# Kernel optimization log

Measured on AMD Instinct MI355X. Metric: run time of the kernel, lower is better.

Reference implementation:

```python
import jax, jax.numpy as jnp
import numpy as np

B, Q, D = 4, 8192, 256
L, P = 2, 8
H0 = W0 = 128
H1 = W1 = 64
EPS = 1e-5


def _bilinear_sample(feat, gx, gy):
    """grid_sample bilinear, padding_mode='border', align_corners=False.
    feat: (B, D, H, W); gx, gy: (B, N) in [-1, 1]. Returns (B, N, D)."""
    b, d, h, w = feat.shape
    # unnormalize (align_corners=False)
    x = ((gx + 1.0) * w - 1.0) * 0.5
    y = ((gy + 1.0) * h - 1.0) * 0.5
    # border padding: clamp coords into valid range
    x = jnp.clip(x, 0.0, w - 1.0)
    y = jnp.clip(y, 0.0, h - 1.0)
    x0 = jnp.floor(x)
    y0 = jnp.floor(y)
    wx = x - x0
    wy = y - y0
    x0i = x0.astype(jnp.int32)
    y0i = y0.astype(jnp.int32)
    x1i = jnp.minimum(x0i + 1, w - 1)
    y1i = jnp.minimum(y0i + 1, h - 1)
    fhw = feat.reshape(b, d, h * w)  # (B, D, H*W)

    def gather(iy, ix):
        idx = iy * w + ix  # (B, N)
        return jnp.take_along_axis(fhw, idx[:, None, :], axis=2)  # (B, D, N)

    v00 = gather(y0i, x0i)
    v01 = gather(y0i, x1i)
    v10 = gather(y1i, x0i)
    v11 = gather(y1i, x1i)
    wxb = wx[:, None, :]
    wyb = wy[:, None, :]
    top = v00 * (1.0 - wxb) + v01 * wxb
    bot = v10 * (1.0 - wxb) + v11 * wxb
    out = top * (1.0 - wyb) + bot * wyb  # (B, D, N)
    return out.transpose(0, 2, 1)  # (B, N, D)


def setup_inputs() -> dict:
    key = jax.random.key(0)
    ks = jax.random.split(key, 12)
    s = 0.02
    return {
        "q": jax.random.normal(ks[0], (B, Q, D), jnp.float32),
        "map0": jax.random.normal(ks[1], (B, D, H0, W0), jnp.float32),
        "map1": jax.random.normal(ks[2], (B, D, H1, W1), jnp.float32),
        "base_ref": jax.random.uniform(ks[3], (B, L, 2), jnp.float32),
        "Wrd": jax.random.normal(ks[4], (D, L * 2), jnp.float32) * s,
        "brd": jax.random.normal(ks[5], (L * 2,), jnp.float32) * s,
        "Woff": jax.random.normal(ks[6], (D, L * P * 2), jnp.float32) * s,
        "boff": jax.random.normal(ks[7], (L * P * 2,), jnp.float32) * 1.5,
        "Wattn": jax.random.normal(ks[8], (D, L * P), jnp.float32) * s,
        "battn": jax.random.normal(ks[9], (L * P,), jnp.float32) * s,
        "Wout": jax.random.normal(ks[10], (D, D), jnp.float32) * s,
        "bout": jax.random.normal(ks[11], (D,), jnp.float32) * s,
    }


def reference(q, map0, map1, base_ref, Wrd, brd, Woff, boff, Wattn, battn, Wout, bout):
    b, qn, d = q.shape
    maps = [map0, map1]
    # per-level reference points, refined through inverse-sigmoid space
    base = jnp.clip(base_ref, EPS, 1.0 - EPS)[:, None, :, :]  # (B, 1, L, 2)
    logit_base = jnp.log(base / (1.0 - base))
    ref_delta = (q @ Wrd + brd).reshape(b, qn, L, 2)
    ref = jax.nn.sigmoid(logit_base + ref_delta)  # (B, Q, L, 2)
    offsets = (q @ Woff + boff).reshape(b, qn, L, P, 2)
    attn_logits = (q @ Wattn + battn).reshape(b, qn, L * P)
    attn = jax.nn.softmax(attn_logits, axis=-1).reshape(b, qn, L, P)

    out = jnp.zeros((b, qn, d), jnp.float32)
    for level, feat in enumerate(maps):
        h, w = feat.shape[2], feat.shape[3]
        normalizer = jnp.array([w, h], jnp.float32)
        loc = ref[:, :, level, None, :] + offsets[:, :, level] / normalizer  # (B,Q,P,2)
        if level == 1:
            loc = jnp.stack([loc[..., 0], jnp.remainder(loc[..., 1], 1.0)], axis=-1)
        loc = loc * 2.0 - 1.0
        gx = loc[..., 0].reshape(b, qn * P)
        gy = loc[..., 1].reshape(b, qn * P)
        samp = _bilinear_sample(feat, gx, gy).reshape(b, qn, P, d)
        out = out + jnp.sum(samp * attn[:, :, level, :, None], axis=2)
    return out @ Wout + bout
```

## Files before the change

kernel.cpp:

```cpp
#include <hip/hip_runtime.h>
#include <hip/hip_bf16.h>

#define BQ 4
#define QN 8192
#define DD 256
#define LL 2
#define H0c 128
#define W0c 128
#define H1c 64
#define W1c 64
#define EPSF 1e-5f

typedef unsigned short ushort_t;
typedef __attribute__((ext_vector_type(8))) short short8;
typedef __attribute__((ext_vector_type(8))) unsigned short ushortx8;
typedef __attribute__((ext_vector_type(4))) unsigned short ushortx4;
typedef __attribute__((ext_vector_type(4))) float floatx4;
typedef __attribute__((ext_vector_type(4))) _Float16 half4;

static __device__ __forceinline__ float lo16f(unsigned int d) {
    union { unsigned int u; float f; } x; x.u = d << 16; return x.f;
}
static __device__ __forceinline__ float hi16f(unsigned int d) {
    union { unsigned int u; float f; } x; x.u = d & 0xFFFF0000u; return x.f;
}
static __device__ __forceinline__ unsigned short f2bf(float f) {
    __hip_bfloat16 h = __float2bfloat16(f);
    return __builtin_bit_cast(unsigned short, h);
}

#define PT0 4096
#define PT1 1024
#define PTW 16
__global__ __launch_bounds__(256) void prep(const float* __restrict__ map0, const float* __restrict__ map1,
                                            const float* __restrict__ Wout,
                                            const float* __restrict__ Wrd, const float* __restrict__ brd,
                                            const float* __restrict__ Woff, const float* __restrict__ boff,
                                            const float* __restrict__ Wattn, const float* __restrict__ battn,
                                            __hip_bfloat16* __restrict__ mapT0, __hip_bfloat16* __restrict__ mapT1,
                                            __hip_bfloat16* __restrict__ WoutT,
                                            float* __restrict__ Wall, float* __restrict__ bias64) {
    __shared__ float tile[64][65];
    int blk = blockIdx.x;
    int tid = threadIdx.x;
    const float* in; __hip_bfloat16* outp; int HW, b, c0, hw0;
    if (blk < PT0) {
        int l = blk; b = l >> 10; int r = l & 1023;
        c0 = (r >> 8) << 6; hw0 = (r & 255) << 6;
        in = map0; outp = mapT0; HW = H0c * W0c;
    } else if (blk < PT0 + PT1) {
        int l = blk - PT0; b = l >> 8; int r = l & 255;
        c0 = (r >> 6) << 6; hw0 = (r & 63) << 6;
        in = map1; outp = mapT1; HW = H1c * W1c;
    } else if (blk < PT0 + PT1 + PTW) {
        int l = blk - PT0 - PT1; b = 0;
        c0 = (l >> 2) << 6; hw0 = (l & 3) << 6;
        in = Wout; outp = WoutT; HW = DD;
    } else {
        int l = blk - PT0 - PT1 - PTW;
        int idx = l * 256 + tid;
        int k = idx >> 6, c = idx & 63;
        float v = (c < 4)  ? Wrd[k * 4 + c]
                : (c < 36) ? Woff[k * 32 + (c - 4)]
                : (c < 52) ? Wattn[k * 16 + (c - 36)]
                : 0.f;
        Wall[idx] = v;
        if (idx < 64) {
            float bv = (idx < 4)  ? brd[idx]
                     : (idx < 36) ? boff[idx - 4]
                     : (idx < 52) ? battn[idx - 36]
                     : 0.f;
            bias64[idx] = bv;
        }
        return;
    }
    const float* inb = in + (size_t)b * DD * HW + (size_t)c0 * HW + hw0;
    __hip_bfloat16* outb = outp + (size_t)b * DD * HW + (size_t)hw0 * DD + c0;

    int row = tid >> 2;
    int q16 = (tid & 3) * 16;
#pragma unroll
    for (int j = 0; j < 4; j++) {
        float4 v = *(const float4*)(inb + (size_t)row * HW + q16 + j * 4);
        tile[row][q16 + j * 4 + 0] = v.x;
        tile[row][q16 + j * 4 + 1] = v.y;
        tile[row][q16 + j * 4 + 2] = v.z;
        tile[row][q16 + j * 4 + 3] = v.w;
    }
    __syncthreads();

    int hwr = tid >> 4;
    int c4 = (tid & 15) * 4;
#pragma unroll
    for (int jj = 0; jj < 4; jj++) {
        int rr = hwr + jj * 16;
        ushortx4 o;
        o[0] = f2bf(tile[c4 + 0][rr]);
        o[1] = f2bf(tile[c4 + 1][rr]);
        o[2] = f2bf(tile[c4 + 2][rr]);
        o[3] = f2bf(tile[c4 + 3][rr]);
        *(ushortx4*)((ushort_t*)outb + (size_t)rr * DD + c4) = o;
    }
}

__global__ __launch_bounds__(256) void proj_desc(const float* __restrict__ q,
                                                 const float* __restrict__ Wall,
                                                 const float* __restrict__ bias64,
                                                 const float* __restrict__ base_ref,
                                                 int2* __restrict__ dsi,
                                                 half4* __restrict__ dsw) {
    __shared__ float As[32][68];
    __shared__ float Bs[32][64];
    __shared__ float prs[64][68];
    int tid = threadIdx.x;
    int tx = tid & 15, ty = tid >> 4;
    int m0 = blockIdx.x * 64;
    float acc[4][4] = {};

    for (int kt = 0; kt < DD; kt += 32) {
#pragma unroll
        for (int j = 0; j < 8; j++) {
            int e = tid + 256 * j;
            int r = e >> 5, k = e & 31;
            As[k][r] = q[(size_t)(m0 + r) * DD + kt + k];
        }
#pragma unroll
        for (int j = 0; j < 8; j++) {
            int e = tid + 256 * j;
            int k = e >> 6, nn = e & 63;
            Bs[k][nn] = Wall[(size_t)(kt + k) * 64 + nn];
        }
        __syncthreads();
#pragma unroll
        for (int k = 0; k < 32; k++) {
            const float4 a4 = *(const float4*)&As[k][ty * 4];
            const float4 b4 = *(const float4*)&Bs[k][tx * 4];
            acc[0][0] += a4.x * b4.x; acc[0][1] += a4.x * b4.y; acc[0][2] += a4.x * b4.z; acc[0][3] += a4.x * b4.w;
            acc[1][0] += a4.y * b4.x; acc[1][1] += a4.y * b4.y; acc[1][2] += a4.y * b4.z; acc[1][3] += a4.y * b4.w;
            acc[2][0] += a4.z * b4.x; acc[2][1] += a4.z * b4.y; acc[2][2] += a4.z * b4.z; acc[2][3] += a4.z * b4.w;
            acc[3][0] += a4.w * b4.x; acc[3][1] += a4.w * b4.y; acc[3][2] += a4.w * b4.z; acc[3][3] += a4.w * b4.w;
        }
        __syncthreads();
    }

    float4 bias = *(const float4*)&bias64[tx * 4];
#pragma unroll
    for (int i = 0; i < 4; i++) {
        float4 v;
        v.x = acc[i][0] + bias.x;
        v.y = acc[i][1] + bias.y;
        v.z = acc[i][2] + bias.z;
        v.w = acc[i][3] + bias.w;
        *(float4*)&prs[ty * 4 + i][tx * 4] = v;
    }
    __syncthreads();

    int ql = tid >> 2, sq = tid & 3;
    int n = m0 + ql, b = n >> 13;
    const float* p = prs[ql];

    float mx = p[36];
#pragma unroll
    for (int i = 1; i < 16; i++) mx = fmaxf(mx, p[36 + i]);
    float sum = 0.f;
#pragma unroll
    for (int i = 0; i < 16; i++) sum += __expf(p[36 + i] - mx);
    float inv = 1.f / sum;

#pragma unroll
    for (int u = 0; u < 4; u++) {
        int s = sq * 4 + u;
        int l = s >> 3;
        float a = __expf(p[36 + s] - mx) * inv;

        int W = l ? W1c : W0c;
        int H = l ? H1c : H0c;
        float Wf = (float)W, Hf = (float)H;

        float bx = base_ref[(b * LL + l) * 2 + 0];
        float by = base_ref[(b * LL + l) * 2 + 1];
        bx = fminf(fmaxf(bx, EPSF), 1.f - EPSF);
        by = fminf(fmaxf(by, EPSF), 1.f - EPSF);
        float lgx = logf(bx / (1.f - bx));
        float lgy = logf(by / (1.f - by));
        float refx = 1.f / (1.f + __expf(-(lgx + p[l * 2 + 0])));
        float refy = 1.f / (1.f + __expf(-(lgy + p[l * 2 + 1])));

        float locx = refx + p[4 + s * 2 + 0] / Wf;
        float locy = refy + p[4 + s * 2 + 1] / Hf;
        if (l == 1) locy = locy - floorf(locy);

        float gx = locx * 2.f - 1.f;
        float gy = locy * 2.f - 1.f;
        float x = ((gx + 1.f) * Wf - 1.f) * 0.5f;
        float y = ((gy + 1.f) * Hf - 1.f) * 0.5f;
        x = fminf(fmaxf(x, 0.f), Wf - 1.f);
        y = fminf(fmaxf(y, 0.f), Hf - 1.f);
        float x0f = floorf(x), y0f = floorf(y);
        float wx = x - x0f, wy = y - y0f;
        int x0 = (int)x0f, y0 = (int)y0f;
        unsigned int dx = (x0 + 1 <= W - 1) ? DD : 0;
        unsigned int dy = (y0 + 1 <= H - 1) ? (unsigned)(W * DD) : 0;
        int base = ((b * H + y0) * W + x0) * DD;

        float omx = 1.f - wx, omy = 1.f - wy;
        half4 w;
        w[0] = (_Float16)(a * omx * omy);
        w[1] = (_Float16)(a * wx  * omy);
        w[2] = (_Float16)(a * omx * wy);
        w[3] = (_Float16)(a * wx  * wy);

        dsi[(size_t)n * 16 + s] = make_int2(base, (int)((dy << 16) | dx));
        dsw[(size_t)n * 16 + s] = w;
    }
}

__global__ __launch_bounds__(256, 3) void sample_kernel(const ushort_t* __restrict__ mapT0,
                                                        const ushort_t* __restrict__ mapT1,
                                                        const int2* __restrict__ dsi,
                                                        const half4* __restrict__ dsw,
                                                        ushort_t* __restrict__ S) {
    int tid = threadIdx.x;
    int lx = tid & 63;
    int n = blockIdx.x * 8 + (tid >> 6) * 2 + (lx >> 5);
    int c8 = (lx & 31) * 8;
    const int2*  gi = dsi + (size_t)n * 16;
    const half4* gw = dsw + (size_t)n * 16;

    int2 g[16]; half4 wh[16];
#pragma unroll
    for (int s = 0; s < 16; s++) { g[s] = gi[s]; wh[s] = gw[s]; }

    float acc[8];
#pragma unroll
    for (int i = 0; i < 8; i++) acc[i] = 0.f;

#pragma unroll
    for (int grp = 0; grp < 4; grp++) {
        const ushort_t* mp = (grp < 2) ? mapT0 : mapT1;
        uint4 u[4][4];
#pragma unroll
        for (int j = 0; j < 4; j++) {
            int s = grp * 4 + j;
            int dx = g[s].y & 0xffff;
            int dy = (int)(((unsigned int)g[s].y) >> 16);
            const ushort_t* p0 = mp + g[s].x + c8;
            u[j][0] = *(const uint4*)(p0);
            u[j][1] = *(const uint4*)(p0 + dx);
            u[j][2] = *(const uint4*)(p0 + dy);
            u[j][3] = *(const uint4*)(p0 + dx + dy);
        }
#pragma unroll
        for (int j = 0; j < 4; j++) {
            int s = grp * 4 + j;
            float w0 = (float)wh[s][0], w1 = (float)wh[s][1], w2 = (float)wh[s][2], w3 = (float)wh[s][3];
#pragma unroll
            for (int corner = 0; corner < 4; corner++) {
                uint4 v = u[j][corner];
                float wc = (corner == 0) ? w0 : (corner == 1) ? w1 : (corner == 2) ? w2 : w3;
                acc[0] += wc * lo16f(v.x); acc[1] += wc * hi16f(v.x);
                acc[2] += wc * lo16f(v.y); acc[3] += wc * hi16f(v.y);
                acc[4] += wc * lo16f(v.z); acc[5] += wc * hi16f(v.z);
                acc[6] += wc * lo16f(v.w); acc[7] += wc * hi16f(v.w);
            }
        }
    }
    ushortx8 o;
#pragma unroll
    for (int i = 0; i < 8; i++) o[i] = f2bf(acc[i]);
    *(ushortx8*)(S + (size_t)n * DD + c8) = o;
}

__global__ __launch_bounds__(256) void out_mfma(const ushort_t* __restrict__ S,
                                                const ushort_t* __restrict__ WT,
                                                const float* __restrict__ bout,
                                                float* __restrict__ out) {
    __shared__ ushort_t wlds[64][256];
    int tid = threadIdx.x;
    int n0c = blockIdx.x * 64;
    int wave = tid >> 6, lane = tid & 63;
    int m0 = blockIdx.y * 64 + wave * 16;
    int mrow = lane & 15, quad = lane >> 4;

#pragma unroll
    for (int i = 0; i < 8; i++) {
        int idx = tid + 256 * i;
        int row = idx >> 5, c = idx & 31;
        *(uint4*)&wlds[row][(c ^ (row & 31)) * 8] =
            *(const uint4*)(WT + (size_t)(n0c + row) * DD + c * 8);
    }
    __syncthreads();

    const ushort_t* Sp = S + (size_t)(m0 + mrow) * DD + quad * 8;
    short8 a[8];
#pragma unroll
    for (int k = 0; k < 8; k++) a[k] = *(const short8*)(Sp + k * 32);

    floatx4 acc[4];
#pragma unroll
    for (int nt = 0; nt < 4; nt++) acc[nt] = {0.f, 0.f, 0.f, 0.f};

#pragma unroll
    for (int nt = 0; nt < 4; nt++) {
        int row = nt * 16 + mrow;
#pragma unroll
        for (int k = 0; k < 8; k++) {
            int c = k * 4 + quad;
            short8 b = *(const short8*)&wlds[row][(c ^ (row & 31)) * 8];
            acc[nt] = __builtin_amdgcn_mfma_f32_16x16x32_bf16(a[k], b, acc[nt], 0, 0, 0);
        }
    }

    int rbase = quad * 4;
#pragma unroll
    for (int nt = 0; nt < 4; nt++) {
        float bv = bout[n0c + nt * 16 + mrow];
#pragma unroll
        for (int r = 0; r < 4; r++) {
            out[(size_t)(m0 + rbase + r) * DD + n0c + nt * 16 + mrow] = acc[nt][r] + bv;
        }
    }
}

extern "C" void kernel_launch(void* const* d_in, const int* in_sizes, int n_in,
                              void* d_out, int out_size, void* d_ws, size_t ws_size,
                              hipStream_t stream) {
    const float* q        = (const float*)d_in[0];
    const float* map0     = (const float*)d_in[1];
    const float* map1     = (const float*)d_in[2];
    const float* base_ref = (const float*)d_in[3];
    const float* Wrd      = (const float*)d_in[4];
    const float* brd      = (const float*)d_in[5];
    const float* Woff     = (const float*)d_in[6];
    const float* boff     = (const float*)d_in[7];
    const float* Wattn    = (const float*)d_in[8];
    const float* battn    = (const float*)d_in[9];
    const float* Wout     = (const float*)d_in[10];
    const float* bout     = (const float*)d_in[11];
    float* out = (float*)d_out;

    char* ws = (char*)d_ws;
    __hip_bfloat16* mapT0  = (__hip_bfloat16*)(ws + 0);
    __hip_bfloat16* mapT1  = (__hip_bfloat16*)(ws + 33554432);
    __hip_bfloat16* WoutT  = (__hip_bfloat16*)(ws + 41943040);
    float*          Wall   = (float*)(ws + 42074112);
    float*          bias64 = (float*)(ws + 42139648);
    int2*           dsi    = (int2*)(ws + 42139904);
    half4*          dsw    = (half4*)(ws + 46334208);
    ushort_t*       Sbuf   = (ushort_t*)(ws + 50528512);

    prep<<<dim3(PT0 + PT1 + PTW + 64), dim3(256), 0, stream>>>(
        map0, map1, Wout, Wrd, brd, Woff, boff, Wattn, battn,
        mapT0, mapT1, WoutT, Wall, bias64);

    proj_desc<<<dim3(BQ * QN / 64), dim3(256), 0, stream>>>(q, Wall, bias64, base_ref, dsi, dsw);

    sample_kernel<<<dim3(BQ * QN / 8), dim3(256), 0, stream>>>(
        (const ushort_t*)mapT0, (const ushort_t*)mapT1, dsi, dsw, Sbuf);

    out_mfma<<<dim3(4, BQ * QN / 64), dim3(256), 0, stream>>>(
        Sbuf, (const ushort_t*)WoutT, bout, out);
}
```

Measured before the change: 245.9 us.

## Merge prep and projection kernels into one launch, store maps as fp16

Folds the projection/descriptor kernel into the map-transpose prep kernel as extra blocks sharing a union of LDS, and reads the projection weights and biases directly instead of packing them into an intermediate buffer first. This drops one kernel launch and the Wall/bias staging pass, and lets projection blocks overlap with transpose blocks. Separately, the transposed feature maps are now stored as fp16 instead of bf16, and the sampler converts from half. The larger union LDS footprint may lower occupancy for the transpose blocks, and fp16 changes rounding and range compared with bf16.

```diff
diff --git a/kernel.cpp b/kernel.cpp
--- a/kernel.cpp
+++ b/kernel.cpp
@@ -18,64 +18,184 @@
 typedef __attribute__((ext_vector_type(4))) float floatx4;
 typedef __attribute__((ext_vector_type(4))) _Float16 half4;
 
-static __device__ __forceinline__ float lo16f(unsigned int d) {
-    union { unsigned int u; float f; } x; x.u = d << 16; return x.f;
-}
-static __device__ __forceinline__ float hi16f(unsigned int d) {
-    union { unsigned int u; float f; } x; x.u = d & 0xFFFF0000u; return x.f;
-}
 static __device__ __forceinline__ unsigned short f2bf(float f) {
     __hip_bfloat16 h = __float2bfloat16(f);
     return __builtin_bit_cast(unsigned short, h);
 }
-
+static __device__ __forceinline__ unsigned short f2h(float f) {
+    _Float16 h = (_Float16)f;
+    return __builtin_bit_cast(unsigned short, h);
+}
+static __device__ __forceinline__ float h_lo(unsigned int u) {
+    _Float16 h = __builtin_bit_cast(_Float16, (unsigned short)(u & 0xffffu));
+    return (float)h;
+}
+static __device__ __forceinline__ float h_hi(unsigned int u) {
+    _Float16 h = __builtin_bit_cast(_Float16, (unsigned short)(u >> 16));
+    return (float)h;
+}
+
+#define PJB 512
 #define PT0 4096
 #define PT1 1024
 #define PTW 16
-__global__ __launch_bounds__(256) void prep(const float* __restrict__ map0, const float* __restrict__ map1,
-                                            const float* __restrict__ Wout,
-                                            const float* __restrict__ Wrd, const float* __restrict__ brd,
-                                            const float* __restrict__ Woff, const float* __restrict__ boff,
-                                            const float* __restrict__ Wattn, const float* __restrict__ battn,
-                                            __hip_bfloat16* __restrict__ mapT0, __hip_bfloat16* __restrict__ mapT1,
-                                            __hip_bfloat16* __restrict__ WoutT,
-                                            float* __restrict__ Wall, float* __restrict__ bias64) {
-    __shared__ float tile[64][65];
+
+union SmemA {
+    struct { float As[32][68]; float Bs[32][64]; float prs[64][68]; } p;
+    float tile[64][65];
+};
+
+__global__ __launch_bounds__(256) void prep_proj(const float* __restrict__ map0, const float* __restrict__ map1,
+                                                 const float* __restrict__ Wout,
+                                                 const float* __restrict__ q,
+                                                 const float* __restrict__ base_ref,
+                                                 const float* __restrict__ Wrd, const float* __restrict__ brd,
+                                                 const float* __restrict__ Woff, const float* __restrict__ boff,
+                                                 const float* __restrict__ Wattn, const float* __restrict__ battn,
+                                                 ushort_t* __restrict__ mapT0, ushort_t* __restrict__ mapT1,
+                                                 __hip_bfloat16* __restrict__ WoutT,
+                                                 int2* __restrict__ dsi, half4* __restrict__ dsw) {
+    __shared__ SmemA sm;
     int blk = blockIdx.x;
     int tid = threadIdx.x;
-    const float* in; __hip_bfloat16* outp; int HW, b, c0, hw0;
-    if (blk < PT0) {
-        int l = blk; b = l >> 10; int r = l & 1023;
+
+    if (blk < PJB) {
+        auto& As  = sm.p.As;
+        auto& Bs  = sm.p.Bs;
+        auto& prs = sm.p.prs;
+        int tx = tid & 15, ty = tid >> 4;
+        int m0 = blk * 64;
+        float acc[4][4] = {};
+
+        for (int kt = 0; kt < DD; kt += 32) {
+#pragma unroll
+            for (int j = 0; j < 8; j++) {
+                int e = tid + 256 * j;
+                int r = e >> 5, k = e & 31;
+                As[k][r] = q[(size_t)(m0 + r) * DD + kt + k];
+            }
+#pragma unroll
+            for (int j = 0; j < 8; j++) {
+                int e = tid + 256 * j;
+                int k = e >> 6, nn = e & 63;
+                int kk = kt + k;
+                float v = (nn < 4)  ? Wrd[kk * 4 + nn]
+                        : (nn < 36) ? Woff[kk * 32 + (nn - 4)]
+                        : (nn < 52) ? Wattn[kk * 16 + (nn - 36)]
+                        : 0.f;
+                Bs[k][nn] = v;
+            }
+            __syncthreads();
+#pragma unroll
+            for (int k = 0; k < 32; k++) {
+                const float4 a4 = *(const float4*)&As[k][ty * 4];
+                const float4 b4 = *(const float4*)&Bs[k][tx * 4];
+                acc[0][0] += a4.x * b4.x; acc[0][1] += a4.x * b4.y; acc[0][2] += a4.x * b4.z; acc[0][3] += a4.x * b4.w;
+                acc[1][0] += a4.y * b4.x; acc[1][1] += a4.y * b4.y; acc[1][2] += a4.y * b4.z; acc[1][3] += a4.y * b4.w;
+                acc[2][0] += a4.z * b4.x; acc[2][1] += a4.z * b4.y; acc[2][2] += a4.z * b4.z; acc[2][3] += a4.z * b4.w;
+                acc[3][0] += a4.w * b4.x; acc[3][1] += a4.w * b4.y; acc[3][2] += a4.w * b4.z; acc[3][3] += a4.w * b4.w;
+            }
+            __syncthreads();
+        }
+
+        float biasv[4];
+#pragma unroll
+        for (int c = 0; c < 4; c++) {
+            int col = tx * 4 + c;
+            biasv[c] = (col < 4)  ? brd[col]
+                     : (col < 36) ? boff[col - 4]
+                     : (col < 52) ? battn[col - 36]
+                     : 0.f;
+        }
+#pragma unroll
+        for (int i = 0; i < 4; i++) {
+            float4 v;
+            v.x = acc[i][0] + biasv[0];
+            v.y = acc[i][1] + biasv[1];
+            v.z = acc[i][2] + biasv[2];
+            v.w = acc[i][3] + biasv[3];
+            *(float4*)&prs[ty * 4 + i][tx * 4] = v;
+        }
+        __syncthreads();
+
+        int ql = tid >> 2, sq = tid & 3;
+        int n = m0 + ql, b = n >> 13;
+        const float* p = prs[ql];
+
+        float mx = p[36];
+#pragma unroll
+        for (int i = 1; i < 16; i++) mx = fmaxf(mx, p[36 + i]);
+        float sum = 0.f;
+#pragma unroll
+        for (int i = 0; i < 16; i++) sum += __expf(p[36 + i] - mx);
+        float inv = 1.f / sum;
+
+#pragma unroll
+        for (int u = 0; u < 4; u++) {
+            int s = sq * 4 + u;
+            int l = s >> 3;
+            float a = __expf(p[36 + s] - mx) * inv;
+
+            int W = l ? W1c : W0c;
+            int H = l ? H1c : H0c;
+            float Wf = (float)W, Hf = (float)H;
+
+            float bx = base_ref[(b * LL + l) * 2 + 0];
+            float by = base_ref[(b * LL + l) * 2 + 1];
+            bx = fminf(fmaxf(bx, EPSF), 1.f - EPSF);
+            by = fminf(fmaxf(by, EPSF), 1.f - EPSF);
+            float lgx = logf(bx / (1.f - bx));
+            float lgy = logf(by / (1.f - by));
+            float refx = 1.f / (1.f + __expf(-(lgx + p[l * 2 + 0])));
+            float refy = 1.f / (1.f + __expf(-(lgy + p[l * 2 + 1])));
+
+            float locx = refx + p[4 + s * 2 + 0] / Wf;
+            float locy = refy + p[4 + s * 2 + 1] / Hf;
+            if (l == 1) locy = locy - floorf(locy);
+
+            float gx = locx * 2.f - 1.f;
+            float gy = locy * 2.f - 1.f;
+            float x = ((gx + 1.f) * Wf - 1.f) * 0.5f;
+            float y = ((gy + 1.f) * Hf - 1.f) * 0.5f;
+            x = fminf(fmaxf(x, 0.f), Wf - 1.f);
+            y = fminf(fmaxf(y, 0.f), Hf - 1.f);
+            float x0f = floorf(x), y0f = floorf(y);
+            float wx = x - x0f, wy = y - y0f;
+            int x0 = (int)x0f, y0 = (int)y0f;
+            unsigned int dx = (x0 + 1 <= W - 1) ? DD : 0;
+            unsigned int dy = (y0 + 1 <= H - 1) ? (unsigned)(W * DD) : 0;
+            int base = ((b * H + y0) * W + x0) * DD;
+
+            float omx = 1.f - wx, omy = 1.f - wy;
+            half4 w;
+            w[0] = (_Float16)(a * omx * omy);
+            w[1] = (_Float16)(a * wx  * omy);
+            w[2] = (_Float16)(a * omx * wy);
+            w[3] = (_Float16)(a * wx  * wy);
+
+            dsi[(size_t)n * 16 + s] = make_int2(base, (int)((dy << 16) | dx));
+            dsw[(size_t)n * 16 + s] = w;
+        }
+        return;
+    }
+
+    auto& tile = sm.tile;
+    const float* in; ushort_t* outp; int HW, b, c0, hw0; bool tohalf;
+    if (blk < PJB + PT0) {
+        int l = blk - PJB; b = l >> 10; int r = l & 1023;
         c0 = (r >> 8) << 6; hw0 = (r & 255) << 6;
-        in = map0; outp = mapT0; HW = H0c * W0c;
-    } else if (blk < PT0 + PT1) {
-        int l = blk - PT0; b = l >> 8; int r = l & 255;
+        in = map0; outp = mapT0; HW = H0c * W0c; tohalf = true;
+    } else if (blk < PJB + PT0 + PT1) {
+        int l = blk - PJB - PT0; b = l >> 8; int r = l & 255;
         c0 = (r >> 6) << 6; hw0 = (r & 63) << 6;
-        in = map1; outp = mapT1; HW = H1c * W1c;
-    } else if (blk < PT0 + PT1 + PTW) {
-        int l = blk - PT0 - PT1; b = 0;
+        in = map1; outp = mapT1; HW = H1c * W1c; tohalf = true;
+    } else {
+        int l = blk - PJB - PT0 - PT1; b = 0;
         c0 = (l >> 2) << 6; hw0 = (l & 3) << 6;
-        in = Wout; outp = WoutT; HW = DD;
-    } else {
-        int l = blk - PT0 - PT1 - PTW;
-        int idx = l * 256 + tid;
-        int k = idx >> 6, c = idx & 63;
-        float v = (c < 4)  ? Wrd[k * 4 + c]
-                : (c < 36) ? Woff[k * 32 + (c - 4)]
-                : (c < 52) ? Wattn[k * 16 + (c - 36)]
-                : 0.f;
-        Wall[idx] = v;
-        if (idx < 64) {
-            float bv = (idx < 4)  ? brd[idx]
-                     : (idx < 36) ? boff[idx - 4]
-                     : (idx < 52) ? battn[idx - 36]
-                     : 0.f;
-            bias64[idx] = bv;
-        }
-        return;
+        in = Wout; outp = (ushort_t*)WoutT; HW = DD; tohalf = false;
     }
     const float* inb = in + (size_t)b * DD * HW + (size_t)c0 * HW + hw0;
-    __hip_bfloat16* outb = outp + (size_t)b * DD * HW + (size_t)hw0 * DD + c0;
+    ushort_t* outb = outp + (size_t)b * DD * HW + (size_t)hw0 * DD + c0;
 
     int row = tid >> 2;
     int q16 = (tid & 3) * 16;
@@ -95,123 +215,18 @@
     for (int jj = 0; jj < 4; jj++) {
         int rr = hwr + jj * 16;
         ushortx4 o;
-        o[0] = f2bf(tile[c4 + 0][rr]);
-        o[1] = f2bf(tile[c4 + 1][rr]);
-        o[2] = f2bf(tile[c4 + 2][rr]);
-        o[3] = f2bf(tile[c4 + 3][rr]);
-        *(ushortx4*)((ushort_t*)outb + (size_t)rr * DD + c4) = o;
-    }
-}
-
-__global__ __launch_bounds__(256) void proj_desc(const float* __restrict__ q,
-                                                 const float* __restrict__ Wall,
-                                                 const float* __restrict__ bias64,
-                                                 const float* __restrict__ base_ref,
-                                                 int2* __restrict__ dsi,
-                                                 half4* __restrict__ dsw) {
-    __shared__ float As[32][68];
-    __shared__ float Bs[32][64];
-    __shared__ float prs[64][68];
-    int tid = threadIdx.x;
-    int tx = tid & 15, ty = tid >> 4;
-    int m0 = blockIdx.x * 64;
-    float acc[4][4] = {};
-
-    for (int kt = 0; kt < DD; kt += 32) {
-#pragma unroll
-        for (int j = 0; j < 8; j++) {
-            int e = tid + 256 * j;
-            int r = e >> 5, k = e & 31;
-            As[k][r] = q[(size_t)(m0 + r) * DD + kt + k];
-        }
-#pragma unroll
-        for (int j = 0; j < 8; j++) {
-            int e = tid + 256 * j;
-            int k = e >> 6, nn = e & 63;
-            Bs[k][nn] = Wall[(size_t)(kt + k) * 64 + nn];
-        }
-        __syncthreads();
-#pragma unroll
-        for (int k = 0; k < 32; k++) {
-            const float4 a4 = *(const float4*)&As[k][ty * 4];
-            const float4 b4 = *(const float4*)&Bs[k][tx * 4];
-            acc[0][0] += a4.x * b4.x; acc[0][1] += a4.x * b4.y; acc[0][2] += a4.x * b4.z; acc[0][3] += a4.x * b4.w;
-            acc[1][0] += a4.y * b4.x; acc[1][1] += a4.y * b4.y; acc[1][2] += a4.y * b4.z; acc[1][3] += a4.y * b4.w;
-            acc[2][0] += a4.z * b4.x; acc[2][1] += a4.z * b4.y; acc[2][2] += a4.z * b4.z; acc[2][3] += a4.z * b4.w;
-            acc[3][0] += a4.w * b4.x; acc[3][1] += a4.w * b4.y; acc[3][2] += a4.w * b4.z; acc[3][3] += a4.w * b4.w;
-        }
-        __syncthreads();
-    }
-
-    float4 bias = *(const float4*)&bias64[tx * 4];
-#pragma unroll
-    for (int i = 0; i < 4; i++) {
-        float4 v;
-        v.x = acc[i][0] + bias.x;
-        v.y = acc[i][1] + bias.y;
-        v.z = acc[i][2] + bias.z;
-        v.w = acc[i][3] + bias.w;
-        *(float4*)&prs[ty * 4 + i][tx * 4] = v;
-    }
-    __syncthreads();
-
-    int ql = tid >> 2, sq = tid & 3;
-    int n = m0 + ql, b = n >> 13;
-    const float* p = prs[ql];
-
-    float mx = p[36];
-#pragma unroll
-    for (int i = 1; i < 16; i++) mx = fmaxf(mx, p[36 + i]);
-    float sum = 0.f;
-#pragma unroll
-    for (int i = 0; i < 16; i++) sum += __expf(p[36 + i] - mx);
-    float inv = 1.f / sum;
-
-#pragma unroll
-    for (int u = 0; u < 4; u++) {
-        int s = sq * 4 + u;
-        int l = s >> 3;
-        float a = __expf(p[36 + s] - mx) * inv;
-
-        int W = l ? W1c : W0c;
-        int H = l ? H1c : H0c;
-        float Wf = (float)W, Hf = (float)H;
-
-        float bx = base_ref[(b * LL + l) * 2 + 0];
-        float by = base_ref[(b * LL + l) * 2 + 1];
-        bx = fminf(fmaxf(bx, EPSF), 1.f - EPSF);
-        by = fminf(fmaxf(by, EPSF), 1.f - EPSF);
-        float lgx = logf(bx / (1.f - bx));
-        float lgy = logf(by / (1.f - by));
-        float refx = 1.f / (1.f + __expf(-(lgx + p[l * 2 + 0])));
-        float refy = 1.f / (1.f + __expf(-(lgy + p[l * 2 + 1])));
-
-        float locx = refx + p[4 + s * 2 + 0] / Wf;
-        float locy = refy + p[4 + s * 2 + 1] / Hf;
-        if (l == 1) locy = locy - floorf(locy);
-
-        float gx = locx * 2.f - 1.f;
-        float gy = locy * 2.f - 1.f;
-        float x = ((gx + 1.f) * Wf - 1.f) * 0.5f;
-        float y = ((gy + 1.f) * Hf - 1.f) * 0.5f;
-        x = fminf(fmaxf(x, 0.f), Wf - 1.f);
-        y = fminf(fmaxf(y, 0.f), Hf - 1.f);
-        float x0f = floorf(x), y0f = floorf(y);
-        float wx = x - x0f, wy = y - y0f;
-        int x0 = (int)x0f, y0 = (int)y0f;
-        unsigned int dx = (x0 + 1 <= W - 1) ? DD : 0;
-        unsigned int dy = (y0 + 1 <= H - 1) ? (unsigned)(W * DD) : 0;
-        int base = ((b * H + y0) * W + x0) * DD;
-
-        float omx = 1.f - wx, omy = 1.f - wy;
-        half4 w;
-        w[0] = (_Float16)(a * omx * omy);
-        w[1] = (_Float16)(a * wx  * omy);
-        w[2] = (_Float16)(a * omx * wy);
-        w[3] = (_Float16)(a * wx  * wy);
-
-        dsi[(size_t)n * 16 + s] = make_int2(base, (int)((dy << 16) | dx));
-        dsw[(size_t)n * 16 + s] = w;
+        if (tohalf) {
+            o[0] = f2h(tile[c4 + 0][rr]);
+            o[1] = f2h(tile[c4 + 1][rr]);
+            o[2] = f2h(tile[c4 + 2][rr]);
+            o[3] = f2h(tile[c4 + 3][rr]);
+        } else {
+            o[0] = f2bf(tile[c4 + 0][rr]);
+            o[1] = f2bf(tile[c4 + 1][rr]);
+            o[2] = f2bf(tile[c4 + 2][rr]);
+            o[3] = f2bf(tile[c4 + 3][rr]);
+        }
+        *(ushortx4*)(outb + (size_t)rr * DD + c4) = o;
     }
 }
 
@@ -258,10 +273,10 @@
             for (int corner = 0; corner < 4; corner++) {
                 uint4 v = u[j][corner];
                 float wc = (corner == 0) ? w0 : (corner == 1) ? w1 : (corner == 2) ? w2 : w3;
-                acc[0] += wc * lo16f(v.x); acc[1] += wc * hi16f(v.x);
-                acc[2] += wc * lo16f(v.y); acc[3] += wc * hi16f(v.y);
-                acc[4] += wc * lo16f(v.z); acc[5] += wc * hi16f(v.z);
-                acc[6] += wc * lo16f(v.w); acc[7] += wc * hi16f(v.w);
+                acc[0] += wc * h_lo(v.x); acc[1] += wc * h_hi(v.x);
+                acc[2] += wc * h_lo(v.y); acc[3] += wc * h_hi(v.y);
+                acc[4] += wc * h_lo(v.z); acc[5] += wc * h_hi(v.z);
+                acc[6] += wc * h_lo(v.w); acc[7] += wc * h_hi(v.w);
             }
         }
     }
@@ -340,23 +355,20 @@
     float* out = (float*)d_out;
 
     char* ws = (char*)d_ws;
-    __hip_bfloat16* mapT0  = (__hip_bfloat16*)(ws + 0);
-    __hip_bfloat16* mapT1  = (__hip_bfloat16*)(ws + 33554432);
+    ushort_t*       mapT0  = (ushort_t*)(ws + 0);
+    ushort_t*       mapT1  = (ushort_t*)(ws + 33554432);
     __hip_bfloat16* WoutT  = (__hip_bfloat16*)(ws + 41943040);
-    float*          Wall   = (float*)(ws + 42074112);
-    float*          bias64 = (float*)(ws + 42139648);
     int2*           dsi    = (int2*)(ws + 42139904);
     half4*          dsw    = (half4*)(ws + 46334208);
     ushort_t*       Sbuf   = (ushort_t*)(ws + 50528512);
 
-    prep<<<dim3(PT0 + PT1 + PTW + 64), dim3(256), 0, stream>>>(
-        map0, map1, Wout, Wrd, brd, Woff, boff, Wattn, battn,
-        mapT0, mapT1, WoutT, Wall, bias64);
-
-    proj_desc<<<dim3(BQ * QN / 64), dim3(256), 0, stream>>>(q, Wall, bias64, base_ref, dsi, dsw);
+    prep_proj<<<dim3(PJB + PT0 + PT1 + PTW), dim3(256), 0, stream>>>(
+        map0, map1, Wout, q, base_ref,
+        Wrd, brd, Woff, boff, Wattn, battn,
+        mapT0, mapT1, WoutT, dsi, dsw);
 
     sample_kernel<<<dim3(BQ * QN / 8), dim3(256), 0, stream>>>(
-        (const ushort_t*)mapT0, (const ushort_t*)mapT1, dsi, dsw, Sbuf);
+        mapT0, mapT1, dsi, dsw, Sbuf);
 
     out_mfma<<<dim3(4, BQ * QN / 64), dim3(256), 0, stream>>>(
         Sbuf, (const ushort_t*)WoutT, bout, out);
```

After: 273.3 us. 1.11x slower.
